# Kernel tuning notes

Measured on AMD Instinct MI355X. Metric: run time of the kernel, lower is better.

Reference implementation:

```python
import jax, jax.numpy as jnp
import numpy as np

N_NODES = 50000
N_EDGES = 800000
F_IN = 64
HEADS = 4
CH = 32
NEG_SLOPE = 0.2  # PyG GATConv default LeakyReLU slope


def gat_conv(x, edge_index, edge_attr, W, att_src, att_dst, We, att_edge, bias):
    """PyG GATConv (concat=True) with edge features and add_self_loops
    (fill_value='mean': self-loop edge_attr = mean of incoming edge_attr)."""
    N = x.shape[0]
    H, C = att_src.shape
    src, dst = edge_index[0], edge_index[1]
    # self-loop edge attributes: scatter-mean of edge_attr by destination
    ones = jnp.ones((src.shape[0],), x.dtype)
    deg = jax.ops.segment_sum(ones, dst, num_segments=N)
    ea_mean = jax.ops.segment_sum(edge_attr, dst, num_segments=N) / jnp.maximum(deg, 1.0)[:, None]
    loop = jnp.arange(N)
    src2 = jnp.concatenate([src, loop])
    dst2 = jnp.concatenate([dst, loop])
    ea2 = jnp.concatenate([edge_attr, ea_mean], axis=0)  # [E+N, F]
    # node / edge projections
    h = (x @ W).reshape(N, H, C)                 # shared lin_src == lin_dst
    a_s = jnp.einsum('nhc,hc->nh', h, att_src)   # [N, H]
    a_d = jnp.einsum('nhc,hc->nh', h, att_dst)
    he = (ea2 @ We).reshape(-1, H, C)            # [E+N, H, C]
    a_e = jnp.einsum('ehc,hc->eh', he, att_edge)
    # per-edge logits + segment softmax over destination neighborhoods
    logits = jax.nn.leaky_relu(a_s[src2] + a_d[dst2] + a_e, NEG_SLOPE)  # [E+N, H]
    m = jax.ops.segment_max(logits, dst2, num_segments=N)
    ex = jnp.exp(logits - m[dst2])
    denom = jax.ops.segment_sum(ex, dst2, num_segments=N)
    alpha = ex / denom[dst2]                     # every node has a self-loop -> denom > 0
    # weighted scatter-add of source messages
    msg = h[src2] * alpha[..., None]             # [E+N, H, C]
    out = jax.ops.segment_sum(msg, dst2, num_segments=N)
    return out.reshape(N, H * C) + bias


def setup_inputs() -> dict:
    key = jax.random.key(0)
    ks = jax.random.split(key, 16)
    s_in = 1.0 / np.sqrt(F_IN)
    s_h = 1.0 / np.sqrt(HEADS * CH)
    return {
        'x': jax.random.normal(ks[0], (N_NODES, F_IN), jnp.float32),
        'edge_attr': jax.random.normal(ks[1], (N_EDGES, F_IN), jnp.float32),
        'W1': jax.random.normal(ks[2], (F_IN, HEADS * CH), jnp.float32) * s_in,
        'as1': jax.random.normal(ks[3], (HEADS, CH), jnp.float32) * s_h,
        'ad1': jax.random.normal(ks[4], (HEADS, CH), jnp.float32) * s_h,
        'We1': jax.random.normal(ks[5], (F_IN, HEADS * CH), jnp.float32) * s_in,
        'ae1': jax.random.normal(ks[6], (HEADS, CH), jnp.float32) * s_h,
        'b1': jnp.zeros((HEADS * CH,), jnp.float32),
        'W2': jax.random.normal(ks[7], (HEADS * CH, HEADS * CH), jnp.float32) * s_h,
        'as2': jax.random.normal(ks[8], (HEADS, CH), jnp.float32) * s_h,
        'ad2': jax.random.normal(ks[9], (HEADS, CH), jnp.float32) * s_h,
        'We2': jax.random.normal(ks[10], (F_IN, HEADS * CH), jnp.float32) * s_in,
        'ae2': jax.random.normal(ks[11], (HEADS, CH), jnp.float32) * s_h,
        'b2': jnp.zeros((HEADS * CH,), jnp.float32),
        'lin_w': jax.random.normal(ks[12], (HEADS * CH, 1), jnp.float32) * s_h,
        'lin_b': jnp.zeros((1,), jnp.float32),
        'edge_index': jax.random.randint(ks[13], (2, N_EDGES), 0, N_NODES, dtype=jnp.int32),
    }


def reference(x, edge_attr, W1, as1, ad1, We1, ae1, b1,
              W2, as2, ad2, We2, ae2, b2, lin_w, lin_b, edge_index):
    h = jax.nn.relu(gat_conv(x, edge_index, edge_attr, W1, as1, ad1, We1, ae1, b1))
    h = gat_conv(h, edge_index, edge_attr, W2, as2, ad2, We2, ae2, b2)
    out = h @ lin_w + lin_b   # [N, 1]
    return out.reshape(-1)
```

## Files before the change

kernel.cpp:

```cpp
#include <hip/hip_runtime.h>
#include <hip/hip_fp16.h>

#define N_NODES 50000
#define N_EDGES 800000
#define F_IN    64
#define HEADS   4
#define CH      32
#define K_DIM   128
#define NEG     0.2f

__device__ __forceinline__ float lrelu(float x) { return x > 0.f ? x : NEG * x; }

__device__ __forceinline__ float h2bits(__half2 h) {
    return *reinterpret_cast<float*>(&h);
}
__device__ __forceinline__ float pick_half(float lo2, float hi2, int head) {
    float f = (head < 2) ? lo2 : hi2;
    __half2 h = *reinterpret_cast<__half2*>(&f);
    return (head & 1) ? __high2float(h) : __low2float(h);
}

__global__ void __launch_bounds__(256)
kc_fold(const int* __restrict__ ei, int* __restrict__ cnt,
        const float* __restrict__ We1, const float* __restrict__ ae1,
        const float* __restrict__ We2, const float* __restrict__ ae2,
        const float* __restrict__ b2,  const float* __restrict__ linw,
        const float* __restrict__ linb,
        float* __restrict__ v, float* __restrict__ cbias) {
    if (blockIdx.x >= N_EDGES / 256) {
        int t = threadIdx.x;
        for (int idx = t; idx < 512; idx += 256) {
            int o = idx >> 6, f = idx & 63;
            const float* We = (o < 4) ? We1 : We2;
            const float* ae = (o < 4) ? ae1 : ae2;
            int h = o & 3;
            float s = 0.f;
            for (int c = 0; c < CH; ++c)
                s += We[f * K_DIM + h * CH + c] * ae[h * CH + c];
            v[o * 64 + f] = s;
        }
        if (t == 0) {
            float s = 0.f;
            for (int k = 0; k < K_DIM; ++k) s += b2[k] * linw[k];
            *cbias = s + linb[0];
        }
        return;
    }
    int e = blockIdx.x * 256 + threadIdx.x;
    atomicAdd(cnt + ei[N_EDGES + e], 1);
}

__global__ void __launch_bounds__(1024)
k2a_bsum(const int* __restrict__ cnt, int* __restrict__ bsum) {
    __shared__ int ws[16];
    int t = threadIdx.x, lane = t & 63, wid = t >> 6;
    int i = blockIdx.x * 1024 + t;
    int v = (i < N_NODES) ? cnt[i] : 0;
#pragma unroll
    for (int m = 1; m < 64; m <<= 1) v += __shfl_xor(v, m, 64);
    if (lane == 0) ws[wid] = v;
    __syncthreads();
    if (t == 0) {
        int s = 0;
#pragma unroll
        for (int k = 0; k < 16; ++k) s += ws[k];
        bsum[blockIdx.x] = s;
    }
}

__global__ void __launch_bounds__(1024)
k2b_scan(const int* __restrict__ cnt, const int* __restrict__ bsum,
         int* __restrict__ starts, int* __restrict__ cursor, int nblk) {
    __shared__ int wsum[16];
    __shared__ int s_off;
    int t = threadIdx.x, lane = t & 63, wid = t >> 6;
    int bid = blockIdx.x;
    if (t == 0) {
        int o = 0;
        for (int b = 0; b < bid; ++b) o += bsum[b];
        s_off = o;
    }
    int i = bid * 1024 + t;
    int v = (i < N_NODES) ? cnt[i] : 0;
    int sc = v;
#pragma unroll
    for (int s = 1; s < 64; s <<= 1) {
        int u = __shfl_up(sc, s, 64);
        if (lane >= s) sc += u;
    }
    if (lane == 63) wsum[wid] = sc;
    __syncthreads();
    if (wid == 0 && lane < 16) {
        int ws = wsum[lane];
#pragma unroll
        for (int s = 1; s < 16; s <<= 1) {
            int u = __shfl_up(ws, s, 64);
            if (lane >= s) ws += u;
        }
        wsum[lane] = ws;
    }
    __syncthreads();
    int off = s_off + ((wid == 0) ? 0 : wsum[wid - 1]);
    int excl = off + sc - v;
    if (i < N_NODES) { starts[i] = excl; cursor[i] = excl; }
    if (bid == nblk - 1 && t == 1023) starts[N_NODES] = s_off + wsum[15];
}

__global__ void __launch_bounds__(256)
k1_edge(const float* __restrict__ ea, const float* __restrict__ v,
        float* __restrict__ aer1, float* __restrict__ aer2) {
    __shared__ float sx[2][32 * 68];
    int t = threadIdx.x;
    int o  = t & 7;
    int le = t >> 3;
    float4 vr[16];
    {
        const float4* vrow = reinterpret_cast<const float4*>(v + o * 64);
#pragma unroll
        for (int c = 0; c < 16; ++c) vr[c] = vrow[c];
    }
    const float4* ea4 = reinterpret_cast<const float4*>(ea);
    int base = blockIdx.x * 256;
    {
        size_t gb = (size_t)base * 16;
        float4 a = ea4[gb + t];
        float4 b = ea4[gb + t + 256];
        int g0 = t, g1 = t + 256;
        *reinterpret_cast<float4*>(&sx[0][(g0 >> 4) * 68 + (g0 & 15) * 4]) = a;
        *reinterpret_cast<float4*>(&sx[0][(g1 >> 4) * 68 + (g1 & 15) * 4]) = b;
    }
    __syncthreads();
    for (int tile = 0; tile < 8; ++tile) {
        float4 a, b;
        if (tile < 7) {
            size_t gb = (size_t)(base + (tile + 1) * 32) * 16;
            a = ea4[gb + t];
            b = ea4[gb + t + 256];
        }
        const float* row = &sx[tile & 1][le * 68];
        float4 ac = make_float4(0.f, 0.f, 0.f, 0.f);
#pragma unroll
        for (int c = 0; c < 16; ++c) {
            float4 x4 = *reinterpret_cast<const float4*>(row + c * 4);
            ac.x = fmaf(x4.x, vr[c].x, ac.x);
            ac.y = fmaf(x4.y, vr[c].y, ac.y);
            ac.z = fmaf(x4.z, vr[c].z, ac.z);
            ac.w = fmaf(x4.w, vr[c].w, ac.w);
        }
        float acc = (ac.x + ac.y) + (ac.z + ac.w);
        int eid = base + tile * 32 + le;
        float* ob = (o < 4) ? aer1 : aer2;
        ob[(size_t)eid * 4 + (o & 3)] = acc;
        if (tile < 7) {
            int g0 = t, g1 = t + 256;
            int nb = (tile + 1) & 1;
            *reinterpret_cast<float4*>(&sx[nb][(g0 >> 4) * 68 + (g0 & 15) * 4]) = a;
            *reinterpret_cast<float4*>(&sx[nb][(g1 >> 4) * 68 + (g1 & 15) * 4]) = b;
        }
        __syncthreads();
    }
}

__global__ void __launch_bounds__(256)
k4_proj1(const float* __restrict__ x, const float* __restrict__ W,
         const float* __restrict__ asf, const float* __restrict__ adf,
         __half* __restrict__ hp, float* __restrict__ asn, float* __restrict__ adn) {
    __shared__ float sxT[F_IN * 33];
    int t = threadIdx.x;
    int n0 = blockIdx.x * 32;
    {
        int f = t & 63, i0 = t >> 6;
#pragma unroll
        for (int s = 0; s < 8; ++s) {
            int i = i0 + s * 4;
            int n = n0 + i;
            sxT[f * 33 + i] = (n < N_NODES) ? x[(size_t)n * F_IN + f] : 0.f;
        }
    }
    __syncthreads();
    int kq = t & 31, nq = t >> 5;
    float acc[4][4] = {};
    for (int f = 0; f < F_IN; ++f) {
        float a0 = sxT[f * 33 + nq * 4 + 0];
        float a1 = sxT[f * 33 + nq * 4 + 1];
        float a2 = sxT[f * 33 + nq * 4 + 2];
        float a3 = sxT[f * 33 + nq * 4 + 3];
        float4 w4 = *reinterpret_cast<const float4*>(W + (size_t)f * K_DIM + kq * 4);
        acc[0][0] += a0 * w4.x; acc[0][1] += a0 * w4.y; acc[0][2] += a0 * w4.z; acc[0][3] += a0 * w4.w;
        acc[1][0] += a1 * w4.x; acc[1][1] += a1 * w4.y; acc[1][2] += a1 * w4.z; acc[1][3] += a1 * w4.w;
        acc[2][0] += a2 * w4.x; acc[2][1] += a2 * w4.y; acc[2][2] += a2 * w4.z; acc[2][3] += a2 * w4.w;
        acc[3][0] += a3 * w4.x; acc[3][1] += a3 * w4.y; acc[3][2] += a3 * w4.z; acc[3][3] += a3 * w4.w;
    }
    int head = kq >> 3;
    float4 va = *reinterpret_cast<const float4*>(asf + kq * 4);
    float4 vd = *reinterpret_cast<const float4*>(adf + kq * 4);
#pragma unroll
    for (int i = 0; i < 4; ++i) {
        int n = n0 + nq * 4 + i;
        if (n < N_NODES) {
            __half2* hp2 = reinterpret_cast<__half2*>(hp + (size_t)n * K_DIM + kq * 4);
            hp2[0] = __float22half2_rn(make_float2(acc[i][0], acc[i][1]));
            hp2[1] = __float22half2_rn(make_float2(acc[i][2], acc[i][3]));
        }
        float s = acc[i][0] * va.x + acc[i][1] * va.y + acc[i][2] * va.z + acc[i][3] * va.w;
        float d = acc[i][0] * vd.x + acc[i][1] * vd.y + acc[i][2] * vd.z + acc[i][3] * vd.w;
#pragma unroll
        for (int m = 1; m < 8; m <<= 1) {
            s += __shfl_xor(s, m, 8);
            d += __shfl_xor(d, m, 8);
        }
        if ((kq & 7) == 0 && n < N_NODES) {
            asn[(size_t)n * 4 + head] = s;
            adn[(size_t)n * 4 + head] = d;
        }
    }
}

__global__ void __launch_bounds__(256)
k3_scatter(const int* __restrict__ ei, const float4* __restrict__ aer1,
           const float4* __restrict__ aer2, const float* __restrict__ asn,
           int* __restrict__ cursor, float4* __restrict__ el) {
    int e = blockIdx.x * 256 + threadIdx.x;
    if (e >= N_EDGES) return;
    int dst = ei[N_EDGES + e];
    int src = ei[e];
    int pos = atomicAdd(cursor + dst, 1);
    float4 a1 = aer1[e];
    float4 a2 = aer2[e];
    float4 as4 = *reinterpret_cast<const float4*>(asn + (size_t)src * 4);
    __half2 sa01 = __float22half2_rn(make_float2(as4.x + a1.x, as4.y + a1.y));
    __half2 sa23 = __float22half2_rn(make_float2(as4.z + a1.z, as4.w + a1.w));
    __half2 e101 = __float22half2_rn(make_float2(a1.x, a1.y));
    __half2 e123 = __float22half2_rn(make_float2(a1.z, a1.w));
    __half2 e201 = __float22half2_rn(make_float2(a2.x, a2.y));
    __half2 e223 = __float22half2_rn(make_float2(a2.z, a2.w));
    float4* r = el + (size_t)pos * 2;
    r[0] = make_float4(__int_as_float(src), h2bits(sa01), h2bits(sa23), h2bits(e101));
    r[1] = make_float4(h2bits(e123), h2bits(e201), h2bits(e223), 0.f);
}

__global__ void __launch_bounds__(256)
k5_agg1(const int* __restrict__ starts, const float* __restrict__ el,
        const float* __restrict__ asn, const float* __restrict__ adn,
        const __half* __restrict__ hp, const float* __restrict__ b1,
        float* __restrict__ x2) {
    int t = threadIdx.x;
    int lane = t & 63;
    int node = blockIdx.x * 4 + (t >> 6);
    if (node >= N_NODES) return;
    int s = starts[node], e = starts[node + 1];
    int head = lane >> 4;
    float adv = adn[(size_t)node * 4 + head];
    float accx = 0.f, accy = 0.f, dsum = 0.f, aesum = 0.f;
    int j = s;
    for (; j + 2 <= e; j += 2) {
        const float* r0 = el + (size_t)j * 8;
        const float* r1 = r0 + 8;
        float4 ra0 = *reinterpret_cast<const float4*>(r0);
        float  rb0 = r0[4];
        float4 ra1 = *reinterpret_cast<const float4*>(r1);
        float  rb1 = r1[4];
        int src0 = __float_as_int(ra0.x);
        int src1 = __float_as_int(ra1.x);
        float sa0 = pick_half(ra0.y, ra0.z, head);
        float sa1 = pick_half(ra1.y, ra1.z, head);
        float ar0 = pick_half(ra0.w, rb0, head);
        float ar1 = pick_half(ra1.w, rb1, head);
        float2 h0 = __half22float2(*reinterpret_cast<const __half2*>(hp + (size_t)src0 * K_DIM + lane * 2));
        float2 h1 = __half22float2(*reinterpret_cast<const __half2*>(hp + (size_t)src1 * K_DIM + lane * 2));
        float ex0 = __expf(lrelu(sa0 + adv));
        float ex1 = __expf(lrelu(sa1 + adv));
        accx = fmaf(ex0, h0.x, fmaf(ex1, h1.x, accx));
        accy = fmaf(ex0, h0.y, fmaf(ex1, h1.y, accy));
        dsum += ex0 + ex1;
        aesum += ar0 + ar1;
    }
    if (j < e) {
        const float* r0 = el + (size_t)j * 8;
        float4 ra0 = *reinterpret_cast<const float4*>(r0);
        float  rb0 = r0[4];
        int src = __float_as_int(ra0.x);
        float sa = pick_half(ra0.y, ra0.z, head);
        float ar = pick_half(ra0.w, rb0, head);
        float ex = __expf(lrelu(sa + adv));
        float2 hv = __half22float2(*reinterpret_cast<const __half2*>(hp + (size_t)src * K_DIM + lane * 2));
        accx = fmaf(ex, hv.x, accx);
        accy = fmaf(ex, hv.y, accy);
        dsum += ex;
        aesum += ar;
    }
    float deg = (float)(e - s);
    float al = aesum / fmaxf(deg, 1.f);
    float exl = __expf(lrelu(asn[(size_t)node * 4 + head] + adv + al));
    float2 hv = __half22float2(*reinterpret_cast<const __half2*>(hp + (size_t)node * K_DIM + lane * 2));
    accx += exl * hv.x;
    accy += exl * hv.y;
    dsum += exl;
    float2 bb = *reinterpret_cast<const float2*>(b1 + lane * 2);
    float2 o;
    o.x = fmaxf(accx / dsum + bb.x, 0.f);
    o.y = fmaxf(accy / dsum + bb.y, 0.f);
    *reinterpret_cast<float2*>(x2 + (size_t)node * K_DIM + lane * 2) = o;
}

__global__ void __launch_bounds__(256)
k6_proj2(const float* __restrict__ x2, const float* __restrict__ W2,
         const float* __restrict__ asf, const float* __restrict__ adf,
         const float* __restrict__ linw,
         float* __restrict__ asg, float* __restrict__ adn) {
    __shared__ float sxT[K_DIM * 33];
    int t = threadIdx.x;
    int n0 = blockIdx.x * 32;
    {
        int f = t & 127, i0 = t >> 7;
#pragma unroll
        for (int s = 0; s < 16; ++s) {
            int i = i0 + s * 2;
            int n = n0 + i;
            sxT[f * 33 + i] = (n < N_NODES) ? x2[(size_t)n * K_DIM + f] : 0.f;
        }
    }
    __syncthreads();
    int kq = t & 31, nq = t >> 5;
    float acc[4][4] = {};
    for (int f = 0; f < K_DIM; ++f) {
        float a0 = sxT[f * 33 + nq * 4 + 0];
        float a1 = sxT[f * 33 + nq * 4 + 1];
        float a2 = sxT[f * 33 + nq * 4 + 2];
        float a3 = sxT[f * 33 + nq * 4 + 3];
        float4 w4 = *reinterpret_cast<const float4*>(W2 + (size_t)f * K_DIM + kq * 4);
        acc[0][0] += a0 * w4.x; acc[0][1] += a0 * w4.y; acc[0][2] += a0 * w4.z; acc[0][3] += a0 * w4.w;
        acc[1][0] += a1 * w4.x; acc[1][1] += a1 * w4.y; acc[1][2] += a1 * w4.z; acc[1][3] += a1 * w4.w;
        acc[2][0] += a2 * w4.x; acc[2][1] += a2 * w4.y; acc[2][2] += a2 * w4.z; acc[2][3] += a2 * w4.w;
        acc[3][0] += a3 * w4.x; acc[3][1] += a3 * w4.y; acc[3][2] += a3 * w4.z; acc[3][3] += a3 * w4.w;
    }
    int head = kq >> 3;
    float4 va = *reinterpret_cast<const float4*>(asf + kq * 4);
    float4 vd = *reinterpret_cast<const float4*>(adf + kq * 4);
    float4 vg = *reinterpret_cast<const float4*>(linw + kq * 4);
#pragma unroll
    for (int i = 0; i < 4; ++i) {
        int n = n0 + nq * 4 + i;
        float s = acc[i][0] * va.x + acc[i][1] * va.y + acc[i][2] * va.z + acc[i][3] * va.w;
        float d = acc[i][0] * vd.x + acc[i][1] * vd.y + acc[i][2] * vd.z + acc[i][3] * vd.w;
        float g = acc[i][0] * vg.x + acc[i][1] * vg.y + acc[i][2] * vg.z + acc[i][3] * vg.w;
#pragma unroll
        for (int m = 1; m < 8; m <<= 1) {
            s += __shfl_xor(s, m, 8);
            d += __shfl_xor(d, m, 8);
            g += __shfl_xor(g, m, 8);
        }
        if ((kq & 7) == 0 && n < N_NODES) {
            asg[(size_t)n * 8 + head] = s;
            asg[(size_t)n * 8 + 4 + head] = g;
            adn[(size_t)n * 4 + head] = d;
        }
    }
}

__global__ void __launch_bounds__(256)
k7_l2(const int* __restrict__ starts, const float* __restrict__ el,
      const float* __restrict__ asg, const float* __restrict__ adn,
      const float* __restrict__ cbias, float* __restrict__ out) {
    int t = threadIdx.x;
    int g16 = t & 15;
    int node = blockIdx.x * 16 + (t >> 4);
    if (node >= N_NODES) return;
    int s = starts[node], e = starts[node + 1];
    float4 ad4 = *reinterpret_cast<const float4*>(adn + (size_t)node * 4);
    float4 dsum = make_float4(0, 0, 0, 0);
    float4 gsum = make_float4(0, 0, 0, 0);
    float4 aesum = make_float4(0, 0, 0, 0);
    for (int j = s + g16; j < e; j += 16) {
        const float* rb = el + (size_t)j * 8;
        int src = __float_as_int(rb[0]);
        float4 r2 = *reinterpret_cast<const float4*>(rb + 4);
        float f5 = r2.y, f6 = r2.z;
        __half2 h01 = *reinterpret_cast<__half2*>(&f5);
        __half2 h23 = *reinterpret_cast<__half2*>(&f6);
        float4 ae4 = make_float4(__low2float(h01), __high2float(h01),
                                 __low2float(h23), __high2float(h23));
        const float* ap = asg + (size_t)src * 8;
        float4 as4 = *reinterpret_cast<const float4*>(ap);
        float4 g4  = *reinterpret_cast<const float4*>(ap + 4);
        float e0 = __expf(lrelu(as4.x + ad4.x + ae4.x));
        float e1 = __expf(lrelu(as4.y + ad4.y + ae4.y));
        float e2 = __expf(lrelu(as4.z + ad4.z + ae4.z));
        float e3 = __expf(lrelu(as4.w + ad4.w + ae4.w));
        dsum.x += e0; dsum.y += e1; dsum.z += e2; dsum.w += e3;
        gsum.x += e0 * g4.x; gsum.y += e1 * g4.y; gsum.z += e2 * g4.z; gsum.w += e3 * g4.w;
        aesum.x += ae4.x; aesum.y += ae4.y; aesum.z += ae4.z; aesum.w += ae4.w;
    }
#pragma unroll
    for (int m = 1; m < 16; m <<= 1) {
        dsum.x += __shfl_xor(dsum.x, m, 16);  dsum.y += __shfl_xor(dsum.y, m, 16);
        dsum.z += __shfl_xor(dsum.z, m, 16);  dsum.w += __shfl_xor(dsum.w, m, 16);
        gsum.x += __shfl_xor(gsum.x, m, 16);  gsum.y += __shfl_xor(gsum.y, m, 16);
        gsum.z += __shfl_xor(gsum.z, m, 16);  gsum.w += __shfl_xor(gsum.w, m, 16);
        aesum.x += __shfl_xor(aesum.x, m, 16); aesum.y += __shfl_xor(aesum.y, m, 16);
        aesum.z += __shfl_xor(aesum.z, m, 16); aesum.w += __shfl_xor(aesum.w, m, 16);
    }
    if (g16 == 0) {
        float deg = fmaxf((float)(e - s), 1.f);
        const float* ap = asg + (size_t)node * 8;
        float4 mas = *reinterpret_cast<const float4*>(ap);
        float4 mg  = *reinterpret_cast<const float4*>(ap + 4);
        float r = cbias[0];
        float e0;
        e0 = __expf(lrelu(mas.x + ad4.x + aesum.x / deg)); r += (gsum.x + e0 * mg.x) / (dsum.x + e0);
        e0 = __expf(lrelu(mas.y + ad4.y + aesum.y / deg)); r += (gsum.y + e0 * mg.y) / (dsum.y + e0);
        e0 = __expf(lrelu(mas.z + ad4.z + aesum.z / deg)); r += (gsum.z + e0 * mg.z) / (dsum.z + e0);
        e0 = __expf(lrelu(mas.w + ad4.w + aesum.w / deg)); r += (gsum.w + e0 * mg.w) / (dsum.w + e0);
        out[node] = r;
    }
}

extern "C" void kernel_launch(void* const* d_in, const int* in_sizes, int n_in,
                              void* d_out, int out_size, void* d_ws, size_t ws_size,
                              hipStream_t stream) {
    (void)in_sizes; (void)n_in; (void)out_size;
    const float* x    = (const float*)d_in[0];
    const float* ea   = (const float*)d_in[1];
    const float* W1   = (const float*)d_in[2];
    const float* as1  = (const float*)d_in[3];
    const float* ad1  = (const float*)d_in[4];
    const float* We1  = (const float*)d_in[5];
    const float* ae1  = (const float*)d_in[6];
    const float* b1   = (const float*)d_in[7];
    const float* W2   = (const float*)d_in[8];
    const float* as2  = (const float*)d_in[9];
    const float* ad2  = (const float*)d_in[10];
    const float* We2  = (const float*)d_in[11];
    const float* ae2  = (const float*)d_in[12];
    const float* b2   = (const float*)d_in[13];
    const float* linw = (const float*)d_in[14];
    const float* linb = (const float*)d_in[15];
    const int*   ei   = (const int*)d_in[16];
    float* out = (float*)d_out;
    float* ws  = (float*)d_ws;

    const int SCAN_BLK = (N_NODES + 1023) / 1024;

    size_t off = 0;
    __half* h1p  = (__half*)(ws + off); off += (size_t)N_NODES * K_DIM / 2;
    float* x2    = ws + off; off += (size_t)N_NODES * K_DIM;
    float* asn1  = ws + off; off += (size_t)N_NODES * 4;
    float* adn1  = ws + off; off += (size_t)N_NODES * 4;
    float* asg2  = ws + off; off += (size_t)N_NODES * 8;
    float* adn2  = ws + off; off += (size_t)N_NODES * 4;
    float* vbuf  = ws + off; off += 512;
    float* cbias = ws + off; off += 64;
    int* starts  = (int*)(ws + off); off += (size_t)N_NODES + 8;
    int* cursor  = (int*)(ws + off); off += (size_t)N_NODES;
    int* bsum    = (int*)(ws + off); off += 64;
    off = (off + 7) & ~(size_t)7;
    float* el    = ws + off; off += (size_t)N_EDGES * 8;
    float* aer1  = ws + off; off += (size_t)N_EDGES * 4;
    float* aer2  = ws + off; off += (size_t)N_EDGES * 4;
    int* cnt     = (int*)(ws + off); off += (size_t)N_NODES;

    if (ws_size < off * sizeof(float)) return;

    hipMemsetAsync(cnt, 0, N_NODES * sizeof(int), stream);

    kc_fold<<<N_EDGES / 256 + 1, 256, 0, stream>>>(ei, cnt, We1, ae1, We2, ae2,
                                                   b2, linw, linb, vbuf, cbias);
    k2a_bsum<<<SCAN_BLK, 1024, 0, stream>>>(cnt, bsum);
    k2b_scan<<<SCAN_BLK, 1024, 0, stream>>>(cnt, bsum, starts, cursor, SCAN_BLK);
    k1_edge<<<N_EDGES / 256, 256, 0, stream>>>(ea, vbuf, aer1, aer2);
    k4_proj1<<<(N_NODES + 31) / 32, 256, 0, stream>>>(x, W1, as1, ad1, h1p, asn1, adn1);
    k3_scatter<<<N_EDGES / 256, 256, 0, stream>>>(ei, (const float4*)aer1, (const float4*)aer2,
                                                  asn1, cursor, (float4*)el);
    k5_agg1<<<(N_NODES + 3) / 4, 256, 0, stream>>>(starts, el, asn1, adn1, h1p, b1, x2);
    k6_proj2<<<(N_NODES + 31) / 32, 256, 0, stream>>>(x2, W2, as2, ad2, linw, asg2, adn2);
    k7_l2<<<(N_NODES + 15) / 16, 256, 0, stream>>>(starts, el, asg2, adn2, cbias, out);
}
```

Measured before the change: 278.8 us.

## Fold layer-2 projection into aggregation and replace cursor atomics with precomputed ranks

Layer-2 only needs the per-head attention scalars and the final linear output, so W2 is folded with att_src, att_dst and lin_w into a 12x128 matrix. That lets the layer-1 aggregation kernel compute those 12 dot products per node straight from shared memory, which removes the x2 buffer write/read and the separate projection kernel. It also records each edge's atomic rank during degree counting, so the scatter kernel computes its position as starts[dst]+rank and needs no second atomic pass. The costs are an extra 800K-int rank buffer, a per-block load of the folded matrix into shared memory, and a small change in float summation order.

Result: faster. 257.8 us (-7.5%).

```diff
diff --git a/kernel.cpp b/kernel.cpp
--- a/kernel.cpp
+++ b/kernel.cpp
@@ -21,12 +21,14 @@
 }
 
 __global__ void __launch_bounds__(256)
-kc_fold(const int* __restrict__ ei, int* __restrict__ cnt,
+kc_fold(const int* __restrict__ ei, int* __restrict__ cnt, int* __restrict__ rank,
         const float* __restrict__ We1, const float* __restrict__ ae1,
         const float* __restrict__ We2, const float* __restrict__ ae2,
+        const float* __restrict__ as2, const float* __restrict__ ad2,
+        const float* __restrict__ W2,
         const float* __restrict__ b2,  const float* __restrict__ linw,
         const float* __restrict__ linb,
-        float* __restrict__ v, float* __restrict__ cbias) {
+        float* __restrict__ v, float* __restrict__ u, float* __restrict__ cbias) {
     if (blockIdx.x >= N_EDGES / 256) {
         int t = threadIdx.x;
         for (int idx = t; idx < 512; idx += 256) {
@@ -39,6 +41,15 @@
                 s += We[f * K_DIM + h * CH + c] * ae[h * CH + c];
             v[o * 64 + f] = s;
         }
+        for (int idx = t; idx < 12 * K_DIM; idx += 256) {
+            int q = idx >> 7, f = idx & 127;
+            int h = q / 3, type = q % 3;
+            const float* w = (type == 0) ? as2 : (type == 1) ? ad2 : linw;
+            float s = 0.f;
+            for (int c = 0; c < CH; ++c)
+                s += W2[(size_t)f * K_DIM + h * CH + c] * w[h * CH + c];
+            u[idx] = s;
+        }
         if (t == 0) {
             float s = 0.f;
             for (int k = 0; k < K_DIM; ++k) s += b2[k] * linw[k];
@@ -47,7 +58,7 @@
         return;
     }
     int e = blockIdx.x * 256 + threadIdx.x;
-    atomicAdd(cnt + ei[N_EDGES + e], 1);
+    rank[e] = atomicAdd(cnt + ei[N_EDGES + e], 1);
 }
 
 __global__ void __launch_bounds__(1024)
@@ -70,7 +81,7 @@
 
 __global__ void __launch_bounds__(1024)
 k2b_scan(const int* __restrict__ cnt, const int* __restrict__ bsum,
-         int* __restrict__ starts, int* __restrict__ cursor, int nblk) {
+         int* __restrict__ starts, int nblk) {
     __shared__ int wsum[16];
     __shared__ int s_off;
     int t = threadIdx.x, lane = t & 63, wid = t >> 6;
@@ -102,7 +113,7 @@
     __syncthreads();
     int off = s_off + ((wid == 0) ? 0 : wsum[wid - 1]);
     int excl = off + sc - v;
-    if (i < N_NODES) { starts[i] = excl; cursor[i] = excl; }
+    if (i < N_NODES) starts[i] = excl;
     if (bid == nblk - 1 && t == 1023) starts[N_NODES] = s_off + wsum[15];
 }
 
@@ -217,14 +228,15 @@
 }
 
 __global__ void __launch_bounds__(256)
-k3_scatter(const int* __restrict__ ei, const float4* __restrict__ aer1,
-           const float4* __restrict__ aer2, const float* __restrict__ asn,
-           int* __restrict__ cursor, float4* __restrict__ el) {
+k3_scatter(const int* __restrict__ ei, const int* __restrict__ rank,
+           const float4* __restrict__ aer1, const float4* __restrict__ aer2,
+           const float* __restrict__ asn, const int* __restrict__ starts,
+           float4* __restrict__ el) {
     int e = blockIdx.x * 256 + threadIdx.x;
     if (e >= N_EDGES) return;
     int dst = ei[N_EDGES + e];
     int src = ei[e];
-    int pos = atomicAdd(cursor + dst, 1);
+    int pos = starts[dst] + rank[e];
     float4 a1 = aer1[e];
     float4 a2 = aer2[e];
     float4 as4 = *reinterpret_cast<const float4*>(asn + (size_t)src * 4);
@@ -240,14 +252,18 @@
 }
 
 __global__ void __launch_bounds__(256)
-k5_agg1(const int* __restrict__ starts, const float* __restrict__ el,
-        const float* __restrict__ asn, const float* __restrict__ adn,
-        const __half* __restrict__ hp, const float* __restrict__ b1,
-        float* __restrict__ x2) {
+k5_fused(const int* __restrict__ starts, const float* __restrict__ el,
+         const float* __restrict__ asn, const float* __restrict__ adn,
+         const __half* __restrict__ hp, const float* __restrict__ b1,
+         const float* __restrict__ u,
+         float* __restrict__ asg, float* __restrict__ adn2) {
+    __shared__ float su[12 * K_DIM];
+    __shared__ float sx2[4 * K_DIM];
     int t = threadIdx.x;
+    for (int i = t; i < 12 * K_DIM; i += 256) su[i] = u[i];
     int lane = t & 63;
-    int node = blockIdx.x * 4 + (t >> 6);
-    if (node >= N_NODES) return;
+    int wv = t >> 6;
+    int node = blockIdx.x * 4 + wv;
     int s = starts[node], e = starts[node + 1];
     int head = lane >> 4;
     float adv = adn[(size_t)node * 4 + head];
@@ -297,63 +313,30 @@
     accy += exl * hv.y;
     dsum += exl;
     float2 bb = *reinterpret_cast<const float2*>(b1 + lane * 2);
-    float2 o;
-    o.x = fmaxf(accx / dsum + bb.x, 0.f);
-    o.y = fmaxf(accy / dsum + bb.y, 0.f);
-    *reinterpret_cast<float2*>(x2 + (size_t)node * K_DIM + lane * 2) = o;
-}
-
-__global__ void __launch_bounds__(256)
-k6_proj2(const float* __restrict__ x2, const float* __restrict__ W2,
-         const float* __restrict__ asf, const float* __restrict__ adf,
-         const float* __restrict__ linw,
-         float* __restrict__ asg, float* __restrict__ adn) {
-    __shared__ float sxT[K_DIM * 33];
-    int t = threadIdx.x;
-    int n0 = blockIdx.x * 32;
-    {
-        int f = t & 127, i0 = t >> 7;
-#pragma unroll
-        for (int s = 0; s < 16; ++s) {
-            int i = i0 + s * 2;
-            int n = n0 + i;
-            sxT[f * 33 + i] = (n < N_NODES) ? x2[(size_t)n * K_DIM + f] : 0.f;
-        }
-    }
-    __syncthreads();
-    int kq = t & 31, nq = t >> 5;
-    float acc[4][4] = {};
-    for (int f = 0; f < K_DIM; ++f) {
-        float a0 = sxT[f * 33 + nq * 4 + 0];
-        float a1 = sxT[f * 33 + nq * 4 + 1];
-        float a2 = sxT[f * 33 + nq * 4 + 2];
-        float a3 = sxT[f * 33 + nq * 4 + 3];
-        float4 w4 = *reinterpret_cast<const float4*>(W2 + (size_t)f * K_DIM + kq * 4);
-        acc[0][0] += a0 * w4.x; acc[0][1] += a0 * w4.y; acc[0][2] += a0 * w4.z; acc[0][3] += a0 * w4.w;
-        acc[1][0] += a1 * w4.x; acc[1][1] += a1 * w4.y; acc[1][2] += a1 * w4.z; acc[1][3] += a1 * w4.w;
-        acc[2][0] += a2 * w4.x; acc[2][1] += a2 * w4.y; acc[2][2] += a2 * w4.z; acc[2][3] += a2 * w4.w;
-        acc[3][0] += a3 * w4.x; acc[3][1] += a3 * w4.y; acc[3][2] += a3 * w4.z; acc[3][3] += a3 * w4.w;
-    }
-    int head = kq >> 3;
-    float4 va = *reinterpret_cast<const float4*>(asf + kq * 4);
-    float4 vd = *reinterpret_cast<const float4*>(adf + kq * 4);
-    float4 vg = *reinterpret_cast<const float4*>(linw + kq * 4);
-#pragma unroll
-    for (int i = 0; i < 4; ++i) {
-        int n = n0 + nq * 4 + i;
-        float s = acc[i][0] * va.x + acc[i][1] * va.y + acc[i][2] * va.z + acc[i][3] * va.w;
-        float d = acc[i][0] * vd.x + acc[i][1] * vd.y + acc[i][2] * vd.z + acc[i][3] * vd.w;
-        float g = acc[i][0] * vg.x + acc[i][1] * vg.y + acc[i][2] * vg.z + acc[i][3] * vg.w;
-#pragma unroll
-        for (int m = 1; m < 8; m <<= 1) {
-            s += __shfl_xor(s, m, 8);
-            d += __shfl_xor(d, m, 8);
-            g += __shfl_xor(g, m, 8);
-        }
-        if ((kq & 7) == 0 && n < N_NODES) {
-            asg[(size_t)n * 8 + head] = s;
-            asg[(size_t)n * 8 + 4 + head] = g;
-            adn[(size_t)n * 4 + head] = d;
+    sx2[wv * K_DIM + lane * 2 + 0] = fmaxf(accx / dsum + bb.x, 0.f);
+    sx2[wv * K_DIM + lane * 2 + 1] = fmaxf(accy / dsum + bb.y, 0.f);
+    __syncthreads();
+    int g = t >> 4;
+    int l16 = t & 15;
+#pragma unroll
+    for (int r = 0; r < 3; ++r) {
+        int oid = g * 3 + r;
+        int nl = oid / 12;
+        int q  = oid % 12;
+        int h = q / 3, type = q % 3;
+        const float* xr = &sx2[nl * K_DIM];
+        const float* ur = &su[q * K_DIM];
+        float sv = 0.f;
+#pragma unroll
+        for (int i = 0; i < 8; ++i)
+            sv = fmaf(xr[l16 + 16 * i], ur[l16 + 16 * i], sv);
+#pragma unroll
+        for (int m = 1; m < 16; m <<= 1) sv += __shfl_xor(sv, m, 16);
+        if (l16 == 0) {
+            int n = blockIdx.x * 4 + nl;
+            if (type == 0)      asg[(size_t)n * 8 + h] = sv;
+            else if (type == 1) adn2[(size_t)n * 4 + h] = sv;
+            else                asg[(size_t)n * 8 + 4 + h] = sv;
         }
     }
 }
@@ -443,16 +426,16 @@
 
     size_t off = 0;
     __half* h1p  = (__half*)(ws + off); off += (size_t)N_NODES * K_DIM / 2;
-    float* x2    = ws + off; off += (size_t)N_NODES * K_DIM;
     float* asn1  = ws + off; off += (size_t)N_NODES * 4;
     float* adn1  = ws + off; off += (size_t)N_NODES * 4;
     float* asg2  = ws + off; off += (size_t)N_NODES * 8;
     float* adn2  = ws + off; off += (size_t)N_NODES * 4;
     float* vbuf  = ws + off; off += 512;
+    float* ubuf  = ws + off; off += 12 * K_DIM;
     float* cbias = ws + off; off += 64;
     int* starts  = (int*)(ws + off); off += (size_t)N_NODES + 8;
-    int* cursor  = (int*)(ws + off); off += (size_t)N_NODES;
     int* bsum    = (int*)(ws + off); off += 64;
+    int* rank    = (int*)(ws + off); off += (size_t)N_EDGES;
     off = (off + 7) & ~(size_t)7;
     float* el    = ws + off; off += (size_t)N_EDGES * 8;
     float* aer1  = ws + off; off += (size_t)N_EDGES * 4;
@@ -463,15 +446,17 @@
 
     hipMemsetAsync(cnt, 0, N_NODES * sizeof(int), stream);
 
-    kc_fold<<<N_EDGES / 256 + 1, 256, 0, stream>>>(ei, cnt, We1, ae1, We2, ae2,
-                                                   b2, linw, linb, vbuf, cbias);
+    kc_fold<<<N_EDGES / 256 + 1, 256, 0, stream>>>(ei, cnt, rank, We1, ae1, We2, ae2,
+                                                   as2, ad2, W2, b2, linw, linb,
+                                                   vbuf, ubuf, cbias);
     k2a_bsum<<<SCAN_BLK, 1024, 0, stream>>>(cnt, bsum);
-    k2b_scan<<<SCAN_BLK, 1024, 0, stream>>>(cnt, bsum, starts, cursor, SCAN_BLK);
+    k2b_scan<<<SCAN_BLK, 1024, 0, stream>>>(cnt, bsum, starts, SCAN_BLK);
     k1_edge<<<N_EDGES / 256, 256, 0, stream>>>(ea, vbuf, aer1, aer2);
     k4_proj1<<<(N_NODES + 31) / 32, 256, 0, stream>>>(x, W1, as1, ad1, h1p, asn1, adn1);
-    k3_scatter<<<N_EDGES / 256, 256, 0, stream>>>(ei, (const float4*)aer1, (const float4*)aer2,
-                                                  asn1, cursor, (float4*)el);
-    k5_agg1<<<(N_NODES + 3) / 4, 256, 0, stream>>>(starts, el, asn1, adn1, h1p, b1, x2);
-    k6_proj2<<<(N_NODES + 31) / 32, 256, 0, stream>>>(x2, W2, as2, ad2, linw, asg2, adn2);
+    k3_scatter<<<N_EDGES / 256, 256, 0, stream>>>(ei, rank, (const float4*)aer1,
+                                                  (const float4*)aer2, asn1, starts,
+                                                  (float4*)el);
+    k5_fused<<<N_NODES / 4, 256, 0, stream>>>(starts, el, asn1, adn1, h1p, b1,
+                                              ubuf, asg2, adn2);
     k7_l2<<<(N_NODES + 15) / 16, 256, 0, stream>>>(starts, el, asg2, adn2, cbias, out);
 }
```
